# Performance work log

Hardware: AMD Instinct MI355X
Metric: run time of the kernel (lower is better)

Reference implementation:

```python
import jax, jax.numpy as jnp
import numpy as np

N, T, I, H = 256, 256, 512, 512

def setup_inputs() -> dict:
    key = jax.random.key(0)
    ks = jax.random.split(key, 9)
    s = 1.0 / np.sqrt(H)  # torch GRUCell init scale
    x = jax.random.normal(ks[0], (N, T, I), jnp.float32)
    is_init = jax.random.bernoulli(ks[1], 0.05, (N, T))  # bool resets
    hx = jax.random.normal(ks[2], (N, T, H), jnp.float32)
    W_ih = jax.random.uniform(ks[3], (3 * H, I), jnp.float32, -s, s)
    W_hh = jax.random.uniform(ks[4], (3 * H, H), jnp.float32, -s, s)
    b_ih = jax.random.uniform(ks[5], (3 * H,), jnp.float32, -s, s)
    b_hh = jax.random.uniform(ks[6], (3 * H,), jnp.float32, -s, s)
    W_out = jax.random.uniform(ks[7], (H, H), jnp.float32, -s, s)
    b_out = jax.random.uniform(ks[8], (H,), jnp.float32, -s, s)
    return {"x": x, "hx": hx, "W_ih": W_ih, "W_hh": W_hh, "b_ih": b_ih,
            "b_hh": b_hh, "W_out": W_out, "b_out": b_out, "is_init": is_init}

def _gru_forward(x, hx, W_ih, W_hh, b_ih, b_hh, W_out, b_out, is_init):
    # recurrent_mode branch; learnable_init=False -> reset to zeros
    mask = is_init[..., None]                         # [N,T,1] bool
    h0 = jnp.where(mask[:, 0], 0.0, hx[:, 0])        # [N,H]
    # precompute input-to-hidden gates for all steps: [N,T,3H]
    xi = jnp.einsum('nti,gi->ntg', x, W_ih) + b_ih

    def step(h, inp):
        xi_t, m_t = inp                              # [N,3H], [N,1]
        h = jnp.where(m_t, 0.0, h)                   # per-step init masking
        hh = h @ W_hh.T + b_hh                       # [N,3H]
        xr, xz, xn = jnp.split(xi_t, 3, axis=-1)
        hr, hz, hn = jnp.split(hh, 3, axis=-1)
        r = jax.nn.sigmoid(xr + hr)
        z = jax.nn.sigmoid(xz + hz)
        n = jnp.tanh(xn + r * hn)
        h_new = (1.0 - z) * n + z * h
        return h_new, h_new

    hT, hs = jax.lax.scan(step, h0,
                          (xi.transpose(1, 0, 2), mask.transpose(1, 0, 2)))
    hs = hs.transpose(1, 0, 2)                       # [N,T,H]
    output = hs @ W_out.T + b_out                    # LazyLinear projection
    hx_out = jnp.broadcast_to(hT[:, None, :], (hT.shape[0], T, hT.shape[1]))
    return output, hx_out

def reference(x, hx, W_ih, W_hh, b_ih, b_hh, W_out, b_out, is_init):
    return _gru_forward(x, hx, W_ih, W_hh, b_ih, b_hh, W_out, b_out, is_init)
```

## Files before the change

### kernel.cpp

```cpp
#include <hip/hip_runtime.h>

#define NB 256
#define TT 256
#define II 512
#define HH 512
#define GG 1536

typedef unsigned short ushort_t;
typedef unsigned int uint_t;
typedef unsigned long long ull_t;
typedef __attribute__((ext_vector_type(8))) short short8;
typedef __attribute__((ext_vector_type(4))) float f32x4;

typedef __attribute__((address_space(3))) void lds_void;
typedef const __attribute__((address_space(1))) void glb_void;

__device__ __forceinline__ ushort_t f2bf(float f) {
  union { float f; unsigned int u; } x; x.f = f;
  unsigned int r = x.u + 0x7FFFu + ((x.u >> 16) & 1u);
  return (ushort_t)(r >> 16);
}
__device__ __forceinline__ float bf2f(ushort_t b) {
  union { unsigned int u; float f; } x; x.u = ((unsigned int)b) << 16;
  return x.f;
}
__device__ __forceinline__ float sigmoidf_(float x) {
  return __fdividef(1.0f, 1.0f + __expf(-x));
}
__device__ __forceinline__ float tanhf_(float x) {
  float t = __expf(2.0f * x);
  return 1.0f - __fdividef(2.0f, t + 1.0f);
}
__device__ __forceinline__ short8 pack8(float4 a, float4 b) {
  short8 r;
  r[0] = (short)f2bf(a.x); r[1] = (short)f2bf(a.y);
  r[2] = (short)f2bf(a.z); r[3] = (short)f2bf(a.w);
  r[4] = (short)f2bf(b.x); r[5] = (short)f2bf(b.y);
  r[6] = (short)f2bf(b.z); r[7] = (short)f2bf(b.w);
  return r;
}

__global__ void mask_detect_kernel(const unsigned char* __restrict__ src,
                                   unsigned char* __restrict__ mask8) {
  __shared__ int fByte, fOdd;
  const int tid = threadIdx.x;
  if (tid == 0) { fByte = 0; fOdd = 0; }
  __syncthreads();
  const uint_t* w = (const uint_t*)src;
  int ab = 0, ao = 0;
  for (int i = tid; i < NB * TT; i += blockDim.x) {
    if ((i & 3) == 1 && src[i]) ab = 1;
    if (i < 16384 && (i & 1) == 1 && w[i]) ao = 1;
  }
  if (ab) fByte = 1;
  if (ao) fOdd = 1;
  __syncthreads();
  const int isByte = fByte, isW32 = fOdd;
  for (int i = tid; i < NB * TT; i += blockDim.x) {
    unsigned char m;
    if (isByte)      m = src[i] ? 1 : 0;
    else if (isW32)  m = w[i] ? 1 : 0;
    else             m = w[2 * i] ? 1 : 0;
    mask8[i] = m;
  }
}

__global__ void cvt_f2bf(const float* __restrict__ src, ushort_t* __restrict__ dst,
                         int n4) {
  int stride = gridDim.x * blockDim.x;
  for (int i = blockIdx.x * blockDim.x + threadIdx.x; i < n4; i += stride) {
    const float4 v = reinterpret_cast<const float4*>(src)[i];
    ushort4 o;
    o.x = f2bf(v.x); o.y = f2bf(v.y); o.z = f2bf(v.z); o.w = f2bf(v.w);
    reinterpret_cast<ushort4*>(dst)[i] = o;
  }
}

__global__ void pack_whh(const float* __restrict__ W, ushort_t* __restrict__ out) {
  int idx = blockIdx.x * blockDim.x + threadIdx.x;
  if (idx >= 96 * 16 * 64) return;
  int l = idx & 63;
  int tk = idx >> 6;
  int tile = tk >> 4, kk = tk & 15;
  int row = tile * 16 + (l & 15);
  int k = kk * 32 + (l >> 4) * 8;
  const float* s = W + (size_t)row * HH + k;
  short8 v;
#pragma unroll
  for (int e = 0; e < 8; ++e) v[e] = (short)f2bf(s[e]);
  *reinterpret_cast<short8*>(out + (size_t)idx * 8) = v;
}

template <int AF32, int CF32>
__global__ __launch_bounds__(256) void gemm_bt(
    const void* __restrict__ Av, const ushort_t* __restrict__ B,
    const float* __restrict__ bias, void* __restrict__ Cv, int NC) {
  __shared__ ushort_t As[128 * 32];
  __shared__ ushort_t Bs[128 * 32];
  const int tid = threadIdx.x;
  const int lane = tid & 63;
  const int w = tid >> 6;
  const int wr = w >> 1, wc = w & 1;
  const int c15 = lane & 15, l4 = lane >> 4;
  const int mbase = blockIdx.x * 128;
  const int nbase = blockIdx.y * 128;

  const int rs = tid >> 2;
  const int kb = (tid & 3) * 8;

  f32x4 acc[4][4] = {};

  const float4* Bg = reinterpret_cast<const float4*>(B);
  auto bIdx = [&](int c, int kt) {
    return ((size_t)(nbase + rs + 64 * c) * 512 + kt * 32 + kb) >> 3;
  };
  float4 rb0 = Bg[bIdx(0, 0)], rb1 = Bg[bIdx(1, 0)];

  const float4* Agf = reinterpret_cast<const float4*>(Av);
  auto aEl = [&](int c, int kt) {
    return (size_t)(mbase + rs + 64 * c) * 512 + kt * 32 + kb;
  };
  float4 a0a, a0b, a1a, a1b;
  float4 h0, h1;
  if constexpr (AF32) {
    a0a = Agf[aEl(0, 0) >> 2]; a0b = Agf[(aEl(0, 0) >> 2) + 1];
    a1a = Agf[aEl(1, 0) >> 2]; a1b = Agf[(aEl(1, 0) >> 2) + 1];
  } else {
    h0 = Agf[aEl(0, 0) >> 3];
    h1 = Agf[aEl(1, 0) >> 3];
  }

  for (int kt = 0; kt < 16; ++kt) {
    __syncthreads();
    if constexpr (AF32) {
      *reinterpret_cast<short8*>(&As[(size_t)tid * 8]) = pack8(a0a, a0b);
      *reinterpret_cast<short8*>(&As[(size_t)(tid + 256) * 8]) = pack8(a1a, a1b);
    } else {
      reinterpret_cast<float4*>(As)[tid] = h0;
      reinterpret_cast<float4*>(As)[tid + 256] = h1;
    }
    reinterpret_cast<float4*>(Bs)[tid] = rb0;
    reinterpret_cast<float4*>(Bs)[tid + 256] = rb1;
    if (kt < 15) {
      if constexpr (AF32) {
        a0a = Agf[aEl(0, kt + 1) >> 2]; a0b = Agf[(aEl(0, kt + 1) >> 2) + 1];
        a1a = Agf[aEl(1, kt + 1) >> 2]; a1b = Agf[(aEl(1, kt + 1) >> 2) + 1];
      } else {
        h0 = Agf[aEl(0, kt + 1) >> 3];
        h1 = Agf[aEl(1, kt + 1) >> 3];
      }
      rb0 = Bg[bIdx(0, kt + 1)]; rb1 = Bg[bIdx(1, kt + 1)];
    }
    __syncthreads();
    short8 af[4], bq[4];
#pragma unroll
    for (int m = 0; m < 4; ++m)
      af[m] = *reinterpret_cast<const short8*>(&As[(wr * 64 + m * 16 + c15) * 32 + l4 * 8]);
#pragma unroll
    for (int n = 0; n < 4; ++n)
      bq[n] = *reinterpret_cast<const short8*>(&Bs[(wc * 64 + n * 16 + c15) * 32 + l4 * 8]);
#pragma unroll
    for (int m = 0; m < 4; ++m)
#pragma unroll
      for (int n = 0; n < 4; ++n)
        acc[m][n] = __builtin_amdgcn_mfma_f32_16x16x32_bf16(af[m], bq[n], acc[m][n], 0, 0, 0);
  }

#pragma unroll
  for (int n = 0; n < 4; ++n) {
    const int col = nbase + wc * 64 + n * 16 + c15;
    const float bv = bias[col];
#pragma unroll
    for (int m = 0; m < 4; ++m) {
      const int row = mbase + wr * 64 + m * 16 + l4 * 4;
#pragma unroll
      for (int q = 0; q < 4; ++q) {
        const float v = acc[m][n][q] + bv;
        if constexpr (CF32)
          reinterpret_cast<float*>(Cv)[(size_t)(row + q) * NC + col] = v;
        else
          reinterpret_cast<ushort_t*>(Cv)[(size_t)(row + q) * NC + col] = f2bf(v);
      }
    }
  }
}

__global__ __launch_bounds__(256, 1) void gru_rec(
    const ushort_t* __restrict__ xi, const ushort_t* __restrict__ Wpk,
    const float* __restrict__ hx, const float* __restrict__ bhh,
    const unsigned char* __restrict__ mask8,
    ushort_t* __restrict__ hs, float* __restrict__ hT,
    char* __restrict__ xch, uint_t* __restrict__ flags) {
  extern __shared__ ushort_t smem[];
  const int HAF_U = 65536, XIL_U = 73728, HST_U = 79872;

  const int tid = threadIdx.x;
  const int lane = tid & 63;
  const int w = tid >> 6;
  const int c15 = lane & 15, l4 = lane >> 4;
  const int bid = blockIdx.x;
  const int a = bid & 7;
  const int b = bid >> 3;
  const int n0 = b * 16;

  const int jl = w * 16 + c15;
  const int jfull = a * 64 + jl;
  const float br = bhh[jfull], bz = bhh[512 + jfull], bn = bhh[1024 + jfull];

  const int wb2 = ((2 * 32 + a * 4 + w) * 16) * 512 + lane * 8;

#pragma unroll
  for (int g = 0; g < 2; ++g)
#pragma unroll
    for (int kk = 0; kk < 16; ++kk)
      __builtin_amdgcn_global_load_lds(
          (glb_void*)(Wpk + ((size_t)((g * 32 + a * 4 + w) * 16 + kk)) * 512 + lane * 8),
          (lds_void*)(smem + w * 16384 + (g * 16 + kk) * 512 + lane * 8), 16, 0, 0);

  size_t xg0, xg1 = 0;
  {
    int c = tid, s = c / 24, r = c % 24, g = r >> 3, p = r & 7;
    xg0 = ((size_t)(n0 + s) * TT) * GG + g * 512 + a * 64 + p * 8;
    if (tid < 128) {
      c = tid + 256; s = c / 24; r = c % 24; g = r >> 3; p = r & 7;
      xg1 = ((size_t)(n0 + s) * TT) * GG + g * 512 + a * 64 + p * 8;
    }
  }
  const int xl0 = tid * 8, xl1 = (tid + 256) * 8;

  char* slot0 = xch + (size_t)(b * 2) * 16384;
  char* slot1 = xch + (size_t)(b * 2 + 1) * 16384;

  const int ps = tid >> 4, po = tid & 15;

  float h[4];
#pragma unroll
  for (int q = 0; q < 4; ++q) {
    const int s = l4 * 4 + q;
    const bool mk0 = mask8[(size_t)(n0 + s) * TT] != 0;
    const float v = mk0 ? 0.0f : hx[((size_t)(n0 + s) * TT) * HH + jfull];
    h[q] = v;
    smem[HST_U + s * 72 + jl] = f2bf(v);
  }
  __syncthreads();
  {
    const ull_t v = *(const ull_t*)(smem + HST_U + ps * 72 + po * 4);
    __hip_atomic_store((ull_t*)(slot0 + ps * 1024 + a * 128 + po * 8), v,
                       __ATOMIC_RELAXED, __HIP_MEMORY_SCOPE_AGENT);
  }
  __syncthreads();
  if (tid == 0)
    __hip_atomic_store(&flags[bid * 32], 1u, __ATOMIC_RELAXED,
                       __HIP_MEMORY_SCOPE_AGENT);

  for (int t = 0; t < TT; ++t) {
    ushort_t* xb = smem + XIL_U + (t & 1) * 3072;
    __builtin_amdgcn_global_load_lds((glb_void*)(xi + xg0 + (size_t)t * GG),
                                     (lds_void*)(xb + xl0), 16, 0, 0);
    if (tid < 128)
      __builtin_amdgcn_global_load_lds((glb_void*)(xi + xg1 + (size_t)t * GG),
                                       (lds_void*)(xb + xl1), 16, 0, 0);

    if (tid < 8) {
      const uint_t tgt = (uint_t)(t + 1);
      while (__hip_atomic_load(&flags[(b * 8 + tid) * 32], __ATOMIC_RELAXED,
                               __HIP_MEMORY_SCOPE_AGENT) < tgt) {}
    }
    __syncthreads();

    const char* src = (t & 1) ? slot1 : slot0;
#pragma unroll
    for (int i = 0; i < 8; ++i) {
      const int c = tid + i * 256;
      const int s = c >> 7, c7 = c & 127;
      const int kk = c7 >> 3, sub = (c >> 1) & 3, e2 = (c & 1) * 8;
      const ull_t v = __hip_atomic_load((const ull_t*)(src + s * 1024 + c7 * 8),
                                        __ATOMIC_RELAXED,
                                        __HIP_MEMORY_SCOPE_AGENT);
      *(ull_t*)((char*)smem + HAF_U * 2 + kk * 1024 +
                ((sub * 256 + s * 16 + e2) ^ ((kk & 7) << 4))) = v;
    }

    const bool domask = (t + 1 < TT);
    const int tn = domask ? (t + 1) : t;
    unsigned char mkv[4];
#pragma unroll
    for (int q = 0; q < 4; ++q)
      mkv[q] = mask8[(size_t)(n0 + l4 * 4 + q) * TT + tn];

    __syncthreads();

    short8 af[16];
#pragma unroll
    for (int kk = 0; kk < 16; ++kk)
      af[kk] = *(const short8*)((char*)smem + HAF_U * 2 + kk * 1024 +
                                ((lane * 16) ^ ((kk & 7) << 4)));

    f32x4 a0 = {0.f, 0.f, 0.f, 0.f}, a1 = a0, a2 = a0;
#pragma unroll
    for (int kk = 0; kk < 16; ++kk) {
      const short8 w0 = *(const short8*)(smem + w * 16384 + kk * 512 + lane * 8);
      const short8 w1 = *(const short8*)(smem + w * 16384 + (16 + kk) * 512 + lane * 8);
      const short8 w2 = *(const short8*)(Wpk + wb2 + kk * 512);
      a0 = __builtin_amdgcn_mfma_f32_16x16x32_bf16(af[kk], w0, a0, 0, 0, 0);
      a1 = __builtin_amdgcn_mfma_f32_16x16x32_bf16(af[kk], w1, a1, 0, 0, 0);
      a2 = __builtin_amdgcn_mfma_f32_16x16x32_bf16(af[kk], w2, a2, 0, 0, 0);
    }

#pragma unroll
    for (int q = 0; q < 4; ++q) {
      const int s = l4 * 4 + q;
      const float xr = bf2f(xb[s * 192 + jl]);
      const float xz = bf2f(xb[s * 192 + 64 + jl]);
      const float xn = bf2f(xb[s * 192 + 128 + jl]);
      const float rr = sigmoidf_(xr + a0[q] + br);
      const float zz = sigmoidf_(xz + a1[q] + bz);
      const float nn = tanhf_(xn + rr * (a2[q] + bn));
      const float hnew = (1.0f - zz) * nn + zz * h[q];
      __builtin_nontemporal_store(
          f2bf(hnew), &hs[((size_t)(n0 + s) * TT + t) * HH + jfull]);
      const float hp = (domask && mkv[q]) ? 0.0f : hnew;
      h[q] = hp;
      smem[HST_U + s * 72 + jl] = f2bf(hp);
    }
    __syncthreads();

    if (domask) {
      char* dst = ((t + 1) & 1) ? slot1 : slot0;
      const ull_t v = *(const ull_t*)(smem + HST_U + ps * 72 + po * 4);
      __hip_atomic_store((ull_t*)(dst + ps * 1024 + a * 128 + po * 8), v,
                         __ATOMIC_RELAXED, __HIP_MEMORY_SCOPE_AGENT);
      __syncthreads();
      if (tid == 0)
        __hip_atomic_store(&flags[bid * 32], (uint_t)(t + 2), __ATOMIC_RELAXED,
                           __HIP_MEMORY_SCOPE_AGENT);
    }
  }

#pragma unroll
  for (int q = 0; q < 4; ++q)
    hT[(size_t)(n0 + l4 * 4 + q) * HH + jfull] = h[q];
}

__global__ void bcast_hT(const float* __restrict__ hT, float* __restrict__ dst) {
  const float4* s = (const float4*)hT;
  float4* d = (float4*)dst;
  const int total = NB * TT * HH / 4;
  const int stride = gridDim.x * blockDim.x;
  for (int c = blockIdx.x * blockDim.x + threadIdx.x; c < total; c += stride) {
    int n = c >> 15;
    int j4 = c & 127;
    d[c] = s[(n << 7) | j4];
  }
}

extern "C" void kernel_launch(void* const* d_in, const int* in_sizes, int n_in,
                              void* d_out, int out_size, void* d_ws, size_t ws_size,
                              hipStream_t stream) {
  const float* x    = (const float*)d_in[0];
  const float* hx   = (const float*)d_in[1];
  const float* Wih  = (const float*)d_in[2];
  const float* Whh  = (const float*)d_in[3];
  const float* bih  = (const float*)d_in[4];
  const float* bhh  = (const float*)d_in[5];
  const float* Wout = (const float*)d_in[6];
  const float* bout = (const float*)d_in[7];
  const unsigned char* isinit = (const unsigned char*)d_in[8];

  char* ws = (char*)d_ws;
  ushort_t* xi    = (ushort_t*)(ws);
  ushort_t* wihb  = (ushort_t*)(ws + 201326592);
  ushort_t* whhp  = (ushort_t*)(ws + 202899456);
  ushort_t* woutb = (ushort_t*)(ws + 204472320);
  unsigned char* mask8 = (unsigned char*)(ws + 204996608);
  float*    hTbuf = (float*)(ws + 205062144);
  uint_t*   flags = (uint_t*)(ws + 205586432);
  char*     xch   = (char*)(ws + 205602816);

  float* out1 = (float*)d_out;
  float* out2 = out1 + (size_t)NB * TT * HH;
  ushort_t* hsb = (ushort_t*)out2;

  hipMemsetAsync(flags, 0, 128 * 32 * sizeof(uint_t), stream);
  mask_detect_kernel<<<1, 1024, 0, stream>>>(isinit, mask8);
  cvt_f2bf<<<768, 256, 0, stream>>>(Wih, wihb, GG * II / 4);
  cvt_f2bf<<<256, 256, 0, stream>>>(Wout, woutb, HH * HH / 4);
  pack_whh<<<384, 256, 0, stream>>>(Whh, whhp);

  dim3 g1(512, 12);
  gemm_bt<1, 0><<<g1, 256, 0, stream>>>((const void*)x, wihb, bih, (void*)xi, GG);

  gru_rec<<<128, 256, 162048, stream>>>(xi, whhp, hx, bhh, mask8, hsb, hTbuf,
                                        xch, flags);

  dim3 g3(512, 4);
  gemm_bt<0, 1><<<g3, 256, 0, stream>>>((const void*)hsb, woutb, bout, (void*)out1, HH);

  bcast_hT<<<2048, 256, 0, stream>>>(hTbuf, out2);
}
```

Baseline: 1.684 ms.

## Publish hidden state in MFMA fragment layout and keep n-gate weights in registers

The third gate's weight slice is now loaded once into 16 short8 registers before the time loop, instead of being re-read from global memory on every step. Producers also write their hidden-state chunk into the exchange buffer already in MFMA A-fragment order. Consumers can then do a linear copy into LDS and read fragments unswizzled, dropping the per-element index and XOR-swizzle math. The tradeoffs are higher register pressure (64 extra VGPRs) and possible LDS bank conflicts now that the swizzle is gone.

Result: no change. 1.669 ms (-0.9%).

```diff
diff --git a/kernel.cpp b/kernel.cpp
--- a/kernel.cpp
+++ b/kernel.cpp
@@ -207,8 +207,6 @@
   const int jfull = a * 64 + jl;
   const float br = bhh[jfull], bz = bhh[512 + jfull], bn = bhh[1024 + jfull];
 
-  const int wb2 = ((2 * 32 + a * 4 + w) * 16) * 512 + lane * 8;
-
 #pragma unroll
   for (int g = 0; g < 2; ++g)
 #pragma unroll
@@ -216,6 +214,12 @@
       __builtin_amdgcn_global_load_lds(
           (glb_void*)(Wpk + ((size_t)((g * 32 + a * 4 + w) * 16 + kk)) * 512 + lane * 8),
           (lds_void*)(smem + w * 16384 + (g * 16 + kk) * 512 + lane * 8), 16, 0, 0);
+
+  const int wb2 = ((2 * 32 + a * 4 + w) * 16) * 512 + lane * 8;
+  short8 wn[16];
+#pragma unroll
+  for (int kk = 0; kk < 16; ++kk)
+    wn[kk] = *(const short8*)(Wpk + wb2 + kk * 512);
 
   size_t xg0, xg1 = 0;
   {
@@ -231,7 +235,10 @@
   char* slot0 = xch + (size_t)(b * 2) * 16384;
   char* slot1 = xch + (size_t)(b * 2 + 1) * 16384;
 
-  const int ps = tid >> 4, po = tid & 15;
+  const int ps = tid >> 4, pj = tid & 15;
+  const int pOff = (2 * a + (pj >> 3)) * 1024 +
+                   (ps + 16 * ((pj >> 1) & 3)) * 16 + (pj & 1) * 8;
+  const int pSrc = HST_U + ps * 72 + pj * 4;
 
   float h[4];
 #pragma unroll
@@ -244,8 +251,8 @@
   }
   __syncthreads();
   {
-    const ull_t v = *(const ull_t*)(smem + HST_U + ps * 72 + po * 4);
-    __hip_atomic_store((ull_t*)(slot0 + ps * 1024 + a * 128 + po * 8), v,
+    const ull_t v = *(const ull_t*)(smem + pSrc);
+    __hip_atomic_store((ull_t*)(slot0 + pOff), v,
                        __ATOMIC_RELAXED, __HIP_MEMORY_SCOPE_AGENT);
   }
   __syncthreads();
@@ -272,13 +279,10 @@
 #pragma unroll
     for (int i = 0; i < 8; ++i) {
       const int c = tid + i * 256;
-      const int s = c >> 7, c7 = c & 127;
-      const int kk = c7 >> 3, sub = (c >> 1) & 3, e2 = (c & 1) * 8;
-      const ull_t v = __hip_atomic_load((const ull_t*)(src + s * 1024 + c7 * 8),
+      const ull_t v = __hip_atomic_load((const ull_t*)(src + c * 8),
                                         __ATOMIC_RELAXED,
                                         __HIP_MEMORY_SCOPE_AGENT);
-      *(ull_t*)((char*)smem + HAF_U * 2 + kk * 1024 +
-                ((sub * 256 + s * 16 + e2) ^ ((kk & 7) << 4))) = v;
+      *(ull_t*)((char*)smem + HAF_U * 2 + c * 8) = v;
     }
 
     const bool domask = (t + 1 < TT);
@@ -293,18 +297,16 @@
     short8 af[16];
 #pragma unroll
     for (int kk = 0; kk < 16; ++kk)
-      af[kk] = *(const short8*)((char*)smem + HAF_U * 2 + kk * 1024 +
-                                ((lane * 16) ^ ((kk & 7) << 4)));
+      af[kk] = *(const short8*)((char*)smem + HAF_U * 2 + kk * 1024 + lane * 16);
 
     f32x4 a0 = {0.f, 0.f, 0.f, 0.f}, a1 = a0, a2 = a0;
 #pragma unroll
     for (int kk = 0; kk < 16; ++kk) {
       const short8 w0 = *(const short8*)(smem + w * 16384 + kk * 512 + lane * 8);
       const short8 w1 = *(const short8*)(smem + w * 16384 + (16 + kk) * 512 + lane * 8);
-      const short8 w2 = *(const short8*)(Wpk + wb2 + kk * 512);
       a0 = __builtin_amdgcn_mfma_f32_16x16x32_bf16(af[kk], w0, a0, 0, 0, 0);
       a1 = __builtin_amdgcn_mfma_f32_16x16x32_bf16(af[kk], w1, a1, 0, 0, 0);
-      a2 = __builtin_amdgcn_mfma_f32_16x16x32_bf16(af[kk], w2, a2, 0, 0, 0);
+      a2 = __builtin_amdgcn_mfma_f32_16x16x32_bf16(af[kk], wn[kk], a2, 0, 0, 0);
     }
 
 #pragma unroll
@@ -327,8 +329,8 @@
 
     if (domask) {
       char* dst = ((t + 1) & 1) ? slot1 : slot0;
-      const ull_t v = *(const ull_t*)(smem + HST_U + ps * 72 + po * 4);
-      __hip_atomic_store((ull_t*)(dst + ps * 1024 + a * 128 + po * 8), v,
+      const ull_t v = *(const ull_t*)(smem + pSrc);
+      __hip_atomic_store((ull_t*)(dst + pOff), v,
                          __ATOMIC_RELAXED, __HIP_MEMORY_SCOPE_AGENT);
       __syncthreads();
       if (tid == 0)
```
